# Optimization experiments

Hardware: AMD Instinct MI355X
Metric: run time of the kernel (lower is better)

## Reference

```python
import jax, jax.numpy as jnp
import numpy as np
from jax import lax

# Geometry derived from calc_block_params_and_padding_1d(32, 1024, 3, 1):
N, H, W, C = 1, 1024, 1024, 64
CO, K = 64, 3
BC = 32        # blocks per spatial dim (bcount)
BS = 34        # input block size (bsize)
BSO = 32       # output block size (bsize_out)
BSTR = 32      # block stride (bstride)
PAD = 1        # pad=2 total -> 1 top/left, 1 bottom/right
M = 512
EPS = 1e-3     # bn_eps


def setup_inputs() -> dict:
    key = jax.random.key(0)
    ks = jax.random.split(key, 8)
    inp_NHWC = jax.random.normal(ks[0], (N, H, W, C), jnp.float32)
    conv_w = jax.random.normal(ks[1], (K, K, C, CO), jnp.float32) * 0.05  # HWIO
    conv_b = jax.random.normal(ks[2], (CO,), jnp.float32) * 0.1
    gamma = 1.0 + 0.1 * jax.random.normal(ks[3], (CO,), jnp.float32)
    beta = 0.1 * jax.random.normal(ks[4], (CO,), jnp.float32)
    running_mean = 0.1 * jax.random.normal(ks[5], (CO,), jnp.float32)
    running_var = jax.random.uniform(ks[6], (CO,), jnp.float32, 0.5, 1.5)
    # active blocks: random subset of the 32x32 block grid, sorted flat ids
    flat = jnp.sort(jax.random.permutation(ks[7], BC * BC)[:M]).astype(jnp.int32)
    active_block_indices = jnp.stack(
        [jnp.zeros((M,), jnp.int32), flat // BC, flat % BC], axis=1)  # (n, i, j)
    return dict(inp_NHWC=inp_NHWC, conv_w=conv_w, conv_b=conv_b, gamma=gamma,
                beta=beta, running_mean=running_mean, running_var=running_var,
                active_block_indices=active_block_indices)


def reference(inp_NHWC, conv_w, conv_b, gamma, beta, running_mean, running_var,
              active_block_indices):
    # pad (as torch F.pad(0,0,1,1,1,1) on NHWC): pad H and W by 1 each side
    x = jnp.pad(inp_NHWC, ((0, 0), (PAD, PAD), (PAD, PAD), (0, 0)))
    n = active_block_indices[:, 0]
    i = active_block_indices[:, 1]
    j = active_block_indices[:, 2]

    # sparse_gather: extract [M, BS, BS, C] active tiles
    def gather(nn, ii, jj):
        return lax.dynamic_slice(x, (nn, ii * BSTR, jj * BSTR, 0), (1, BS, BS, C))[0]
    p = jax.vmap(gather)(n, i, j)  # [M, 34, 34, C]

    # conv (VALID, stride 1) + inference BatchNorm + ReLU
    q = lax.conv_general_dilated(p, conv_w, (1, 1), 'VALID',
                                 dimension_numbers=('NHWC', 'HWIO', 'NHWC'))
    q = q + conv_b
    scale = gamma * lax.rsqrt(running_var + EPS)
    q = jnp.maximum(q * scale + (beta - running_mean * scale), 0.0)  # [M, 32, 32, CO]

    # sparse_scatter (add=False): blocks tile the output exactly (BSO == BSTR)
    out6 = jnp.zeros((N, BC, BSO, BC, BSO, CO), inp_NHWC.dtype)
    out6 = out6.at[n, i, :, j].set(q)  # advanced idx -> [M, BSO, BSO, CO]
    return out6.reshape(N, BC * BSO, BC * BSO, CO)
```

## Files before the change

kernel.cpp:

```cpp
#include <hip/hip_runtime.h>

typedef _Float16 f16;
typedef f16 f16x8 __attribute__((ext_vector_type(8)));
typedef float f32x16 __attribute__((ext_vector_type(16)));

#define IMG_H 1024
#define IMG_W 1024
#define CIN 64
#define COUT_ 64
#define NBLK 32
#define NACT 512
#define EPS_ 1e-3f

#define WT_ELEMS (36 * 2 * 64 * 8)

__global__ void prep_weights_k(const float* __restrict__ w, f16* __restrict__ wt) {
    int t = blockIdx.x * 256 + threadIdx.x;
    if (t >= WT_ELEMS) return;
    int j  = t & 7;
    int l  = (t >> 3) & 63;
    int ch = (t >> 9) & 1;
    int ks = t >> 10;
    int tap = ks >> 2, q = ks & 3;
    int ky = tap / 3, kx = tap % 3;
    int cin  = q * 16 + ((l >> 5) << 3) + j;
    int cout = ch * 32 + (l & 31);
    wt[t] = (f16)w[((ky * 3 + kx) * CIN + cin) * COUT_ + cout];
}

__launch_bounds__(256, 2)
__global__ void fused_k(const float* __restrict__ inp,
                        const f16*  __restrict__ wt,
                        const float* __restrict__ cb,
                        const float* __restrict__ gamma,
                        const float* __restrict__ beta,
                        const float* __restrict__ rmean,
                        const float* __restrict__ rvar,
                        const int*  __restrict__ abi,
                        float* __restrict__ out) {
    __shared__ uint4 lds[18 * 34 * 8];
    __shared__ int act;

    const int wg = blockIdx.x;
    const int tid = threadIdx.x;

    if (wg >= 2 * NACT) {
        int b  = wg - 2 * NACT;
        int bi = b >> 5, bj = b & 31;
        if (tid == 0) act = 0;
        __syncthreads();
        int e0 = 2 * tid, e1 = 2 * tid + 1;
        if (abi[3 * e0 + 1] == bi && abi[3 * e0 + 2] == bj) act = 1;
        if (abi[3 * e1 + 1] == bi && abi[3 * e1 + 2] == bj) act = 1;
        __syncthreads();
        if (act) return;
        float4 z = make_float4(0.f, 0.f, 0.f, 0.f);
        float4* base = (float4*)(out + ((size_t)(bi * 32) * IMG_W + bj * 32) * COUT_);
        for (int it = tid; it < 32 * 512; it += 256) {
            int r  = it >> 9;
            int c4 = it & 511;
            base[(size_t)r * (IMG_W * COUT_ / 4) + c4] = z;
        }
        return;
    }

    const int ab = wg >> 1, yh = wg & 1;
    const int bi = abi[3 * ab + 1];
    const int bj = abi[3 * ab + 2];
    const int lane = tid & 63;
    const int wv   = tid >> 6;

    const int r0 = bi * 32 + yh * 16 - 1;
    const int c0 = bj * 32 - 1;
    for (int task = tid; task < 18 * 34 * 8; task += 256) {
        int g  = task & 7;
        int p  = task >> 3;
        int dr = p / 34;
        int dc = p - dr * 34;
        int row = r0 + dr, col = c0 + dc;
        float4 a = make_float4(0.f, 0.f, 0.f, 0.f), b = a;
        if ((unsigned)row < IMG_H && (unsigned)col < IMG_W) {
            const float4* src = (const float4*)(inp + (((size_t)row * IMG_W + col) * CIN + g * 8));
            a = src[0]; b = src[1];
        }
        f16x8 v;
        v[0] = (f16)a.x; v[1] = (f16)a.y; v[2] = (f16)a.z; v[3] = (f16)a.w;
        v[4] = (f16)b.x; v[5] = (f16)b.y; v[6] = (f16)b.z; v[7] = (f16)b.w;
        lds[(p << 3) + (g ^ (dc & 7))] = __builtin_bit_cast(uint4, v);
    }

    const int rg  = wv & 1;
    const int chh = wv >> 1;
    f16x8 wf[36];
    const uint4* wt4 = (const uint4*)wt;
    #pragma unroll
    for (int ks = 0; ks < 36; ++ks)
        wf[ks] = __builtin_bit_cast(f16x8, wt4[(ks * 2 + chh) * 64 + lane]);

    const int co = chh * 32 + (lane & 31);
    const float sc = gamma[co] * rsqrtf(rvar[co] + EPS_);
    const float sh = cb[co] * sc + beta[co] - rmean[co] * sc;

    __syncthreads();

    const int px = lane & 31;
    const int hi = lane >> 5;
    float* outb = out + (((size_t)(bi * 32 + yh * 16) * IMG_W) + bj * 32) * COUT_;

    for (int yr = 0; yr < 8; ++yr) {
        const int R = rg * 8 + yr;
        f32x16 accA = {0.f,0.f,0.f,0.f,0.f,0.f,0.f,0.f,0.f,0.f,0.f,0.f,0.f,0.f,0.f,0.f};
        f32x16 accB = {0.f,0.f,0.f,0.f,0.f,0.f,0.f,0.f,0.f,0.f,0.f,0.f,0.f,0.f,0.f,0.f};
        #pragma unroll
        for (int ks = 0; ks < 36; ++ks) {
            const int tap = ks >> 2, q = ks & 3;
            const int ky = tap / 3, kx = tap % 3;
            const int dr = R + ky;
            const int dc = px + kx;
            const int slot = (q * 2 + hi) ^ (dc & 7);
            uint4 a = lds[((dr * 34 + dc) << 3) + slot];
            if (ks & 1)
                accB = __builtin_amdgcn_mfma_f32_32x32x16_f16(__builtin_bit_cast(f16x8, a), wf[ks], accB, 0, 0, 0);
            else
                accA = __builtin_amdgcn_mfma_f32_32x32x16_f16(__builtin_bit_cast(f16x8, a), wf[ks], accA, 0, 0, 0);
        }
        #pragma unroll
        for (int r = 0; r < 16; ++r) {
            const int pxo = (r & 3) + 8 * (r >> 2) + 4 * hi;
            float v = fmaxf((accA[r] + accB[r]) * sc + sh, 0.f);
            outb[((size_t)R * IMG_W + pxo) * COUT_ + co] = v;
        }
    }
}

extern "C" void kernel_launch(void* const* d_in, const int* in_sizes, int n_in,
                              void* d_out, int out_size, void* d_ws, size_t ws_size,
                              hipStream_t stream) {
    const float* inp   = (const float*)d_in[0];
    const float* convw = (const float*)d_in[1];
    const float* convb = (const float*)d_in[2];
    const float* gamma = (const float*)d_in[3];
    const float* beta  = (const float*)d_in[4];
    const float* rmean = (const float*)d_in[5];
    const float* rvar  = (const float*)d_in[6];
    const int*   abi   = (const int*)d_in[7];
    float* out = (float*)d_out;

    f16* wt = (f16*)d_ws;

    hipLaunchKernelGGL(prep_weights_k, dim3((WT_ELEMS + 255) / 256), dim3(256), 0, stream, convw, wt);
    hipLaunchKernelGGL(fused_k, dim3(2 * NACT + NBLK * NBLK), dim3(256), 0, stream,
                       inp, wt, convb, gamma, beta, rmean, rvar, abi, out);
}
```

Before: 108.8 us.

## Split active blocks into quarter tiles, precompute active flags, interleave zero-fill workgroups

Active blocks are now split into four 8-row quarters instead of two halves, which shrinks the LDS tile and raises launch bounds to three workgroups per CU. A prep kernel builds an active-block flag array, so zero-fill workgroups do a single lookup instead of scanning all indices. Zero-fill and compute workgroups are interleaved in the grid to balance load, and output stores become nontemporal. The trade-off is more halo reloading (10 rows per 8 output rows) and more weight-fragment loads per output.

```diff
diff --git a/kernel.cpp b/kernel.cpp
--- a/kernel.cpp
+++ b/kernel.cpp
@@ -3,6 +3,7 @@
 typedef _Float16 f16;
 typedef f16 f16x8 __attribute__((ext_vector_type(8)));
 typedef float f32x16 __attribute__((ext_vector_type(16)));
+typedef float f32x4v __attribute__((ext_vector_type(4)));
 
 #define IMG_H 1024
 #define IMG_W 1024
@@ -13,10 +14,24 @@
 #define EPS_ 1e-3f
 
 #define WT_ELEMS (36 * 2 * 64 * 8)
+#define WT_WGS   144
+#define FLAGS_OFF (WT_ELEMS * 2)
 
-__global__ void prep_weights_k(const float* __restrict__ w, f16* __restrict__ wt) {
-    int t = blockIdx.x * 256 + threadIdx.x;
-    if (t >= WT_ELEMS) return;
+__global__ void prep_k(const float* __restrict__ w, const int* __restrict__ abi,
+                       f16* __restrict__ wt, int* __restrict__ flags) {
+    int wg = blockIdx.x;
+    if (wg == WT_WGS) {
+        int tid = threadIdx.x;
+        for (int i = tid; i < NBLK * NBLK; i += 256) flags[i] = 0;
+        __syncthreads();
+        for (int t = tid; t < NACT; t += 256) {
+            int bi = abi[3 * t + 1];
+            int bj = abi[3 * t + 2];
+            flags[bi * NBLK + bj] = 1;
+        }
+        return;
+    }
+    int t = wg * 256 + threadIdx.x;
     int j  = t & 7;
     int l  = (t >> 3) & 63;
     int ch = (t >> 9) & 1;
@@ -28,7 +43,7 @@
     wt[t] = (f16)w[((ky * 3 + kx) * CIN + cin) * COUT_ + cout];
 }
 
-__launch_bounds__(256, 2)
+__launch_bounds__(256, 3)
 __global__ void fused_k(const float* __restrict__ inp,
                         const f16*  __restrict__ wt,
                         const float* __restrict__ cb,
@@ -37,42 +52,39 @@
                         const float* __restrict__ rmean,
                         const float* __restrict__ rvar,
                         const int*  __restrict__ abi,
+                        const int*  __restrict__ flags,
                         float* __restrict__ out) {
-    __shared__ uint4 lds[18 * 34 * 8];
-    __shared__ int act;
+    __shared__ uint4 lds[10 * 34 * 8];
 
-    const int wg = blockIdx.x;
+    const int wg  = blockIdx.x;
     const int tid = threadIdx.x;
+    const int r3  = wg % 3;
+    const int z3  = wg / 3;
 
-    if (wg >= 2 * NACT) {
-        int b  = wg - 2 * NACT;
+    if (r3 == 1) {
+        int b = z3;
+        if (flags[b]) return;
         int bi = b >> 5, bj = b & 31;
-        if (tid == 0) act = 0;
-        __syncthreads();
-        int e0 = 2 * tid, e1 = 2 * tid + 1;
-        if (abi[3 * e0 + 1] == bi && abi[3 * e0 + 2] == bj) act = 1;
-        if (abi[3 * e1 + 1] == bi && abi[3 * e1 + 2] == bj) act = 1;
-        __syncthreads();
-        if (act) return;
-        float4 z = make_float4(0.f, 0.f, 0.f, 0.f);
-        float4* base = (float4*)(out + ((size_t)(bi * 32) * IMG_W + bj * 32) * COUT_);
+        f32x4v z = {0.f, 0.f, 0.f, 0.f};
+        f32x4v* base = (f32x4v*)(out + ((size_t)(bi * 32) * IMG_W + bj * 32) * COUT_);
         for (int it = tid; it < 32 * 512; it += 256) {
             int r  = it >> 9;
             int c4 = it & 511;
-            base[(size_t)r * (IMG_W * COUT_ / 4) + c4] = z;
+            __builtin_nontemporal_store(z, &base[(size_t)r * (IMG_W * COUT_ / 4) + c4]);
         }
         return;
     }
 
-    const int ab = wg >> 1, yh = wg & 1;
+    const int ci = 2 * z3 + (r3 >> 1);
+    const int ab = ci >> 2, qt = ci & 3;
     const int bi = abi[3 * ab + 1];
     const int bj = abi[3 * ab + 2];
     const int lane = tid & 63;
     const int wv   = tid >> 6;
 
-    const int r0 = bi * 32 + yh * 16 - 1;
+    const int r0 = bi * 32 + qt * 8 - 1;
     const int c0 = bj * 32 - 1;
-    for (int task = tid; task < 18 * 34 * 8; task += 256) {
+    for (int task = tid; task < 10 * 34 * 8; task += 256) {
         int g  = task & 7;
         int p  = task >> 3;
         int dr = p / 34;
@@ -105,10 +117,10 @@
 
     const int px = lane & 31;
     const int hi = lane >> 5;
-    float* outb = out + (((size_t)(bi * 32 + yh * 16) * IMG_W) + bj * 32) * COUT_;
+    float* outb = out + (((size_t)(bi * 32 + qt * 8) * IMG_W) + bj * 32) * COUT_;
 
-    for (int yr = 0; yr < 8; ++yr) {
-        const int R = rg * 8 + yr;
+    for (int yr = 0; yr < 4; ++yr) {
+        const int R = rg * 4 + yr;
         f32x16 accA = {0.f,0.f,0.f,0.f,0.f,0.f,0.f,0.f,0.f,0.f,0.f,0.f,0.f,0.f,0.f,0.f};
         f32x16 accB = {0.f,0.f,0.f,0.f,0.f,0.f,0.f,0.f,0.f,0.f,0.f,0.f,0.f,0.f,0.f,0.f};
         #pragma unroll
@@ -128,7 +140,7 @@
         for (int r = 0; r < 16; ++r) {
             const int pxo = (r & 3) + 8 * (r >> 2) + 4 * hi;
             float v = fmaxf((accA[r] + accB[r]) * sc + sh, 0.f);
-            outb[((size_t)R * IMG_W + pxo) * COUT_ + co] = v;
+            __builtin_nontemporal_store(v, &outb[((size_t)R * IMG_W + pxo) * COUT_ + co]);
         }
     }
 }
@@ -146,9 +158,10 @@
     const int*   abi   = (const int*)d_in[7];
     float* out = (float*)d_out;
 
-    f16* wt = (f16*)d_ws;
+    f16* wt    = (f16*)d_ws;
+    int* flags = (int*)((char*)d_ws + FLAGS_OFF);
 
-    hipLaunchKernelGGL(prep_weights_k, dim3((WT_ELEMS + 255) / 256), dim3(256), 0, stream, convw, wt);
-    hipLaunchKernelGGL(fused_k, dim3(2 * NACT + NBLK * NBLK), dim3(256), 0, stream,
-                       inp, wt, convb, gamma, beta, rmean, rvar, abi, out);
+    hipLaunchKernelGGL(prep_k, dim3(WT_WGS + 1), dim3(256), 0, stream, convw, abi, wt, flags);
+    hipLaunchKernelGGL(fused_k, dim3(3 * NBLK * NBLK), dim3(256), 0, stream,
+                       inp, wt, convb, gamma, beta, rmean, rvar, abi, flags, out);
 }
```

New measurement: 138.4 us. 1.27x slower.
